# Performance work log

Hardware: AMD Instinct MI355X
Metric: run time of the kernel (lower is better)

Reference implementation:

```python
import jax, jax.numpy as jnp
import numpy as np
from jax.scipy.special import logsumexp

B, S, T = 512, 512, 78  # batch, seq_len, num_tags (num_types=78 in SatoModel)


def setup_inputs() -> dict:
    key = jax.random.key(0)
    k1, k2, k3, k4, k5 = jax.random.split(key, 5)
    emissions = jax.random.normal(k1, (B, S, T), dtype=jnp.float32)
    mask = jax.random.randint(k2, (B, S), 0, 2).astype(bool)
    start_transitions = jax.random.normal(k3, (T,), dtype=jnp.float32)
    end_transitions = jax.random.normal(k4, (T,), dtype=jnp.float32)
    transitions = jax.random.normal(k5, (T, T), dtype=jnp.float32)
    return {
        "emissions": emissions,
        "mask": mask,
        "start_transitions": start_transitions,
        "end_transitions": end_transitions,
        "transitions": transitions,
    }


def reference(emissions, mask, start_transitions, end_transitions, transitions):
    # CRF.forward: partition - score
    # score: masked forward algorithm (note: this CRF's _compute_score never uses
    # gold tags; it is a masked logsumexp DP, reproduced faithfully).
    # partition: unmasked forward algorithm (its where(mask, a, a) is a no-op).
    init = start_transitions[None, :] + emissions[:, 0]  # [B, T]

    ems = jnp.moveaxis(emissions[:, 1:], 1, 0)  # [S-1, B, T]
    msk = jnp.moveaxis(mask[:, 1:], 1, 0)       # [S-1, B]

    def dp_step(state, em_i):
        # state: [B, T]; transitions: [T, T]; em_i: [B, T]
        return logsumexp(state[:, :, None] + transitions[None, :, :] + em_i[:, None, :], axis=1)

    def step(carry, inp):
        score, alpha = carry
        em_i, m_i = inp
        next_score = dp_step(score, em_i)
        score = jnp.where(m_i[:, None], next_score, score)
        alpha = dp_step(alpha, em_i)
        return (score, alpha), None

    (score, alpha), _ = jax.lax.scan(step, (init, init), (ems, msk))

    score_final = logsumexp(score + end_transitions[None, :], axis=1)      # [B]
    partition = logsumexp(alpha + end_transitions[None, :], axis=1)        # [B]
    return partition - score_final
```

## Files before the change

### kernel.cpp

```cpp
#include <hip/hip_runtime.h>

#define BB 512
#define SS 512
#define TT 78
#define TP 80
#define NT 128

typedef float v2f __attribute__((ext_vector_type(2)));
typedef float v4f __attribute__((ext_vector_type(4)));

__device__ __forceinline__ float fexp(float x) { return __expf(x); }
__device__ __forceinline__ float flog(float x) { return __logf(x); }

template<int I> struct ic { static constexpr int v = I; };
template<int I, int N, typename F>
__device__ __forceinline__ void sfor(F f) {
    if constexpr (I < N) {
        f(ic<I>{});
        sfor<I + 1, N>(f);
    }
}

__global__ __launch_bounds__(NT, 1) void crf_fwd_kernel(
    const float* __restrict__ em,
    const unsigned int* __restrict__ mi32,
    const float* __restrict__ st,
    const float* __restrict__ en_,
    const float* __restrict__ tr,
    float* __restrict__ out)
{
    const int b    = blockIdx.x;
    const int tid  = threadIdx.x;
    const int wid  = tid >> 6;
    const int lane = tid & 63;
    const bool has2 = lane < (TT - 64);
    const int t0  = lane;
    const int t1  = lane + 64;
    const int t1c = has2 ? t1 : (TT - 1);

    __shared__ __align__(16) float sE[2][TP];
    __shared__ float sfin[2];
    __shared__ int sflag;

    if (tid == 0) sflag = 1;
    __syncthreads();
    {
        bool okl = true;
        for (int k = tid; k < 512; k += NT) okl = okl && (mi32[k] <= 1u);
        if (!okl) atomicAnd(&sflag, 0);
    }
    __syncthreads();
    const bool mask_int = (sflag != 0);
    const unsigned char* mi8 = (const unsigned char*)mi32;
    const bool is_alpha = (wid == 1);

    v2f et0[TP / 2];
    v2f et1[TP / 2];
    sfor<0, TP / 2>([&](auto P) {
        constexpr int p  = decltype(P)::v;
        constexpr int j0 = 2 * p, j1 = 2 * p + 1;
        float a0v = (j0 < TT) ? fexp(tr[j0 * TT + t0])  : 0.0f;
        float a1v = (j1 < TT) ? fexp(tr[j1 * TT + t0])  : 0.0f;
        float b0v = (j0 < TT) ? fexp(tr[j0 * TT + t1c]) : 0.0f;
        float b1v = (j1 < TT) ? fexp(tr[j1 * TT + t1c]) : 0.0f;
        et0[p] = (v2f){a0v, a1v};
        et1[p] = (v2f){b0v, b1v};
    });

    const size_t base = (size_t)b * SS * TT;
    float sc0 = st[t0] + em[base + t0];
    float sc1 = st[t1c] + em[base + t1c];

    if (lane == 14 || lane == 15) sE[wid][64 + lane] = 0.f;

    const float* rp = em + base + TT;
    float en0 = rp[t0];
    float en1 = rp[t1c];
    unsigned int mk_n = mask_int ? mi32[b * SS + 1] : (unsigned int)mi8[b * SS + 1];

    for (int i = 1; i < SS; ++i) {
        float m = __builtin_amdgcn_readfirstlane(sc0);
        sE[wid][lane] = fexp(sc0 - m);
        if (has2) sE[wid][64 + lane] = fexp(sc1 - m);

        const float emi0 = en0, emi1 = en1;
        const unsigned int mki = mk_n;
        if (i + 1 < SS) {
            rp += TT;
            en0 = rp[t0];
            en1 = rp[t1c];
            mk_n = mask_int ? mi32[b * SS + i + 1] : (unsigned int)mi8[b * SS + i + 1];
        }
        __builtin_amdgcn_wave_barrier();

        const v4f* ep = (const v4f*)sE[wid];
        v4f xs[TP / 4];
        sfor<0, TP / 4>([&](auto K) {
            constexpr int k = decltype(K)::v;
            xs[k] = ep[k];
        });

        v2f a0 = {0.f, 0.f}, a1 = {0.f, 0.f};
        v2f c0 = {0.f, 0.f}, c1 = {0.f, 0.f};
        sfor<0, TP / 4>([&](auto K) {
            constexpr int k = decltype(K)::v;
            v2f xlo = {xs[k].x, xs[k].y};
            v2f xhi = {xs[k].z, xs[k].w};
            a0 = __builtin_elementwise_fma(xlo, et0[2 * k + 0], a0);
            a1 = __builtin_elementwise_fma(xhi, et0[2 * k + 1], a1);
            c0 = __builtin_elementwise_fma(xlo, et1[2 * k + 0], c0);
            c1 = __builtin_elementwise_fma(xhi, et1[2 * k + 1], c1);
        });
        v2f va = a0 + a1;
        v2f vc = c0 + c1;
        float v0 = va.x + va.y;
        float v1 = vc.x + vc.y;

        float nsc0 = emi0 + m + flog(v0);
        float nsc1 = emi1 + m + flog(v1);
        const bool upd = is_alpha | (mki != 0);
        sc0 = upd ? nsc0 : sc0;
        sc1 = upd ? nsc1 : sc1;
    }

    float f0 = sc0 + en_[t0];
    float f1 = has2 ? (sc1 + en_[t1c]) : -1e30f;
    float mm = fmaxf(f0, f1);
    #pragma unroll
    for (int o = 32; o > 0; o >>= 1) mm = fmaxf(mm, __shfl_xor(mm, o));
    float s = fexp(f0 - mm) + (has2 ? fexp(f1 - mm) : 0.f);
    #pragma unroll
    for (int o = 32; o > 0; o >>= 1) s += __shfl_xor(s, o);
    if (lane == 0) sfin[wid] = mm + flog(s);
    __syncthreads();
    if (tid == 0) out[b] = sfin[1] - sfin[0];
}

extern "C" void kernel_launch(void* const* d_in, const int* in_sizes, int n_in,
                              void* d_out, int out_size, void* d_ws, size_t ws_size,
                              hipStream_t stream) {
    const float* emissions    = (const float*)d_in[0];
    const unsigned int* mask  = (const unsigned int*)d_in[1];
    const float* start_trans  = (const float*)d_in[2];
    const float* end_trans    = (const float*)d_in[3];
    const float* transitions  = (const float*)d_in[4];
    float* out = (float*)d_out;

    crf_fwd_kernel<<<BB, NT, 0, stream>>>(emissions, mask, start_trans,
                                          end_trans, transitions, out);
}
```

Before: 239.1 us.

## Run CRF recursion in scaled linear space with power-of-two renormalization

The forward recursion now keeps exp-domain state and multiplies by precomputed exp(emission) each step, removing the per-element exp and log from the serial loop. It renormalizes by a power of two taken from the first lane's exponent bits and tracks the accumulated exponent as an integer. Two batches are packed per 256-thread block, and a large LDS pad array limits occupancy to one block per CU. The risk is overflow or underflow when values within a row span a wide dynamic range, and the fixed occupancy may leave CUs underused.

```diff
diff --git a/kernel.cpp b/kernel.cpp
--- a/kernel.cpp
+++ b/kernel.cpp
@@ -1,139 +1,136 @@
 #include <hip/hip_runtime.h>
 
-#define BB 512
+#define BB 256
 #define SS 512
 #define TT 78
 #define TP 80
-#define NT 128
+#define NT 256
 
 typedef float v2f __attribute__((ext_vector_type(2)));
 typedef float v4f __attribute__((ext_vector_type(4)));
 
-__device__ __forceinline__ float fexp(float x) { return __expf(x); }
-__device__ __forceinline__ float flog(float x) { return __logf(x); }
-
 template<int I> struct ic { static constexpr int v = I; };
 template<int I, int N, typename F>
 __device__ __forceinline__ void sfor(F f) {
-    if constexpr (I < N) {
-        f(ic<I>{});
-        sfor<I + 1, N>(f);
-    }
+    if constexpr (I < N) { f(ic<I>{}); sfor<I + 1, N>(f); }
 }
 
-__global__ __launch_bounds__(NT, 1) void crf_fwd_kernel(
-    const float* __restrict__ em,
-    const unsigned int* __restrict__ mi32,
-    const float* __restrict__ st,
-    const float* __restrict__ en_,
-    const float* __restrict__ tr,
-    float* __restrict__ out)
+__global__ __attribute__((amdgpu_flat_work_group_size(NT, NT)))
+void crf_fwd_kernel(const float* __restrict__ em,
+                    const unsigned int* __restrict__ mi32,
+                    const float* __restrict__ st,
+                    const float* __restrict__ en_,
+                    const float* __restrict__ tr,
+                    float* __restrict__ out)
 {
-    const int b    = blockIdx.x;
+    __shared__ __align__(16) float sE[4][TP];
+    __shared__ float sfin[4];
+    __shared__ int sflag;
+    __shared__ char lds_pad[84 * 1024];
+
     const int tid  = threadIdx.x;
-    const int wid  = tid >> 6;
+    const int w    = tid >> 6;
     const int lane = tid & 63;
-    const bool has2 = lane < (TT - 64);
-    const int t0  = lane;
-    const int t1  = lane + 64;
-    const int t1c = has2 ? t1 : (TT - 1);
+    ((volatile char*)lds_pad)[tid] = 0;
 
-    __shared__ __align__(16) float sE[2][TP];
-    __shared__ float sfin[2];
-    __shared__ int sflag;
+    const int  batch    = blockIdx.x * 2 + (w >> 1);
+    const bool is_alpha = (w & 1) != 0;
+    const bool has2     = lane < (TT - 64);
+    const int  t0  = lane;
+    const int  t1c = has2 ? (lane + 64) : (TT - 1);
 
     if (tid == 0) sflag = 1;
     __syncthreads();
-    {
-        bool okl = true;
-        for (int k = tid; k < 512; k += NT) okl = okl && (mi32[k] <= 1u);
-        if (!okl) atomicAnd(&sflag, 0);
-    }
+    { bool ok = true;
+      for (int k = tid; k < 512; k += NT) ok = ok && (mi32[k] <= 1u);
+      if (!ok) atomicAnd(&sflag, 0); }
     __syncthreads();
     const bool mask_int = (sflag != 0);
     const unsigned char* mi8 = (const unsigned char*)mi32;
-    const bool is_alpha = (wid == 1);
 
-    v2f et0[TP / 2];
-    v2f et1[TP / 2];
+    v2f et0[TP / 2], et1[TP / 2];
     sfor<0, TP / 2>([&](auto P) {
-        constexpr int p  = decltype(P)::v;
+        constexpr int p = decltype(P)::v;
         constexpr int j0 = 2 * p, j1 = 2 * p + 1;
-        float a0v = (j0 < TT) ? fexp(tr[j0 * TT + t0])  : 0.0f;
-        float a1v = (j1 < TT) ? fexp(tr[j1 * TT + t0])  : 0.0f;
-        float b0v = (j0 < TT) ? fexp(tr[j0 * TT + t1c]) : 0.0f;
-        float b1v = (j1 < TT) ? fexp(tr[j1 * TT + t1c]) : 0.0f;
+        float a0v = (j0 < TT) ? __expf(tr[j0 * TT + t0])  : 0.f;
+        float a1v = (j1 < TT) ? __expf(tr[j1 * TT + t0])  : 0.f;
+        float b0v = (j0 < TT) ? __expf(tr[j0 * TT + t1c]) : 0.f;
+        float b1v = (j1 < TT) ? __expf(tr[j1 * TT + t1c]) : 0.f;
+        asm volatile("" : "+v"(a0v), "+v"(a1v), "+v"(b0v), "+v"(b1v));
         et0[p] = (v2f){a0v, a1v};
         et1[p] = (v2f){b0v, b1v};
     });
 
-    const size_t base = (size_t)b * SS * TT;
-    float sc0 = st[t0] + em[base + t0];
-    float sc1 = st[t1c] + em[base + t1c];
+    const size_t base = (size_t)batch * SS * TT;
+    float e0 = __expf(st[t0]  + em[base + t0]);
+    float e1 = __expf(st[t1c] + em[base + t1c]);
+    int M2 = 0;
 
-    if (lane == 14 || lane == 15) sE[wid][64 + lane] = 0.f;
+    if (lane == 14 || lane == 15) sE[w][64 + lane] = 0.f;
+    sE[w][lane] = e0;
+    if (has2) sE[w][64 + lane] = e1;
 
     const float* rp = em + base + TT;
-    float en0 = rp[t0];
-    float en1 = rp[t1c];
-    unsigned int mk_n = mask_int ? mi32[b * SS + 1] : (unsigned int)mi8[b * SS + 1];
+    float EmN0 = __expf(rp[t0]);
+    float EmN1 = __expf(rp[t1c]);
+    unsigned int mk_n = mask_int ? mi32[batch * SS + 1]
+                                 : (unsigned int)mi8[batch * SS + 1];
 
     for (int i = 1; i < SS; ++i) {
-        float m = __builtin_amdgcn_readfirstlane(sc0);
-        sE[wid][lane] = fexp(sc0 - m);
-        if (has2) sE[wid][64 + lane] = fexp(sc1 - m);
-
-        const float emi0 = en0, emi1 = en1;
+        const float Em0 = EmN0, Em1 = EmN1;
         const unsigned int mki = mk_n;
         if (i + 1 < SS) {
             rp += TT;
-            en0 = rp[t0];
-            en1 = rp[t1c];
-            mk_n = mask_int ? mi32[b * SS + i + 1] : (unsigned int)mi8[b * SS + i + 1];
+            EmN0 = __expf(rp[t0]);
+            EmN1 = __expf(rp[t1c]);
+            mk_n = mask_int ? mi32[batch * SS + i + 1]
+                            : (unsigned int)mi8[batch * SS + i + 1];
         }
         __builtin_amdgcn_wave_barrier();
 
-        const v4f* ep = (const v4f*)sE[wid];
+        const v4f* ep = (const v4f*)sE[w];
         v4f xs[TP / 4];
+        sfor<0, TP / 4>([&](auto K) { constexpr int k = decltype(K)::v; xs[k] = ep[k]; });
+
+        v2f a0{0,0}, a1{0,0}, c0{0,0}, c1{0,0};
         sfor<0, TP / 4>([&](auto K) {
             constexpr int k = decltype(K)::v;
-            xs[k] = ep[k];
-        });
-
-        v2f a0 = {0.f, 0.f}, a1 = {0.f, 0.f};
-        v2f c0 = {0.f, 0.f}, c1 = {0.f, 0.f};
-        sfor<0, TP / 4>([&](auto K) {
-            constexpr int k = decltype(K)::v;
-            v2f xlo = {xs[k].x, xs[k].y};
-            v2f xhi = {xs[k].z, xs[k].w};
-            a0 = __builtin_elementwise_fma(xlo, et0[2 * k + 0], a0);
+            v2f xlo = {xs[k].x, xs[k].y}, xhi = {xs[k].z, xs[k].w};
+            a0 = __builtin_elementwise_fma(xlo, et0[2 * k],     a0);
             a1 = __builtin_elementwise_fma(xhi, et0[2 * k + 1], a1);
-            c0 = __builtin_elementwise_fma(xlo, et1[2 * k + 0], c0);
+            c0 = __builtin_elementwise_fma(xlo, et1[2 * k],     c0);
             c1 = __builtin_elementwise_fma(xhi, et1[2 * k + 1], c1);
         });
-        v2f va = a0 + a1;
-        v2f vc = c0 + c1;
+        v2f va = a0 + a1, vc = c0 + c1;
         float v0 = va.x + va.y;
         float v1 = vc.x + vc.y;
 
-        float nsc0 = emi0 + m + flog(v0);
-        float nsc1 = emi1 + m + flog(v1);
+        float vref = __builtin_amdgcn_readfirstlane(v0);
+        int   d2   = (int)((__float_as_uint(vref) >> 23) & 0xFF) - 127;
+        float scl  = __uint_as_float((unsigned)(127 - d2) << 23);
+        float n0 = v0 * scl * Em0;
+        float n1 = v1 * scl * Em1;
+
         const bool upd = is_alpha | (mki != 0);
-        sc0 = upd ? nsc0 : sc0;
-        sc1 = upd ? nsc1 : sc1;
+        e0 = upd ? n0 : e0;
+        e1 = upd ? n1 : e1;
+        M2 = upd ? M2 + d2 : M2;
+
+        __builtin_amdgcn_wave_barrier();
+        sE[w][lane] = e0;
+        if (has2) sE[w][64 + lane] = e1;
     }
 
-    float f0 = sc0 + en_[t0];
-    float f1 = has2 ? (sc1 + en_[t1c]) : -1e30f;
-    float mm = fmaxf(f0, f1);
+    float fs = e0 * __expf(en_[t0]);
+    if (has2) fs += e1 * __expf(en_[t1c]);
     #pragma unroll
-    for (int o = 32; o > 0; o >>= 1) mm = fmaxf(mm, __shfl_xor(mm, o));
-    float s = fexp(f0 - mm) + (has2 ? fexp(f1 - mm) : 0.f);
-    #pragma unroll
-    for (int o = 32; o > 0; o >>= 1) s += __shfl_xor(s, o);
-    if (lane == 0) sfin[wid] = mm + flog(s);
+    for (int o = 32; o > 0; o >>= 1) fs += __shfl_xor(fs, o);
+    if (lane == 0) sfin[w] = __logf(fs) + (float)M2 * 0.6931471805599453f;
     __syncthreads();
-    if (tid == 0) out[b] = sfin[1] - sfin[0];
+    if (tid == 0) {
+        out[blockIdx.x * 2 + 0] = sfin[1] - sfin[0];
+        out[blockIdx.x * 2 + 1] = sfin[3] - sfin[2];
+    }
 }
 
 extern "C" void kernel_launch(void* const* d_in, const int* in_sizes, int n_in,
```

New measurement: 201.1 us. -15.9%, faster.
